# Optimization experiments

Measured on AMD Instinct MI355X. Metric: run time of the kernel, lower is better.

The kernel has to match this reference:

```python
import jax, jax.numpy as jnp
import numpy as np

B, T, C, H = 16, 2048, 768, 128

def setup_inputs() -> dict:
    key = jax.random.key(0)
    k1, k2, k3, k4 = jax.random.split(key, 4)
    x = jax.random.normal(k1, (B, T, C), dtype=jnp.float32)
    Wq = jax.random.normal(k2, (C, H), dtype=jnp.float32) * (C ** -0.5)
    Wk = jax.random.normal(k3, (C, H), dtype=jnp.float32) * (C ** -0.5)
    Wv = jax.random.normal(k4, (C, H), dtype=jnp.float32) * (C ** -0.5)
    return {"x": x, "Wq": Wq, "Wk": Wk, "Wv": Wv}

def reference(x, Wq, Wk, Wv):
    Bc, Tc, Cc = x.shape
    q = jnp.einsum('btc,ch->bth', x, Wq)
    k = jnp.einsum('btc,ch->bth', x, Wk)
    v = jnp.einsum('btc,ch->bth', x, Wv)
    wei = jnp.einsum('bqh,bkh->bqk', q, k)  # [B,T,T]
    tril = jnp.tril(jnp.ones((Tc, Tc), dtype=jnp.float32))
    # Faithful to original: mask with -inf FIRST, then scale by C**-0.5
    wei = jnp.where(tril == 0, -jnp.inf, wei) * (Cc ** -0.5)
    wei = jax.nn.softmax(wei, axis=-1)
    out = jnp.einsum('bqk,bkh->bqh', wei, v)
    return out
```

## Files before the change

kernel.cpp:

```cpp
#include <hip/hip_runtime.h>
#include <hip/hip_bf16.h>
#include <cstdint>

#define B_ 16
#define T_ 2048
#define C_ 768
#define H_ 128

typedef __bf16 bf16x8 __attribute__((ext_vector_type(8)));
typedef float f32x4 __attribute__((ext_vector_type(4)));
typedef float f32x16 __attribute__((ext_vector_type(16)));
typedef unsigned short u16x8 __attribute__((ext_vector_type(8)));
typedef unsigned int u32x4 __attribute__((ext_vector_type(4)));

__device__ __forceinline__ void gld_lds16(const void* g, void* s) {
    __builtin_amdgcn_global_load_lds(
        (__attribute__((address_space(1))) void*)(size_t)g,
        (__attribute__((address_space(3))) void*)s,
        16, 0, 0);
}

__device__ __forceinline__ unsigned short f2bf(float f) {
    __bf16 h = (__bf16)f;
    return __builtin_bit_cast(unsigned short, h);
}

__global__ __launch_bounds__(256) void wconv_kernel(
    const float* __restrict__ Wq, const float* __restrict__ Wk,
    const float* __restrict__ Wv, unsigned short* __restrict__ wT) {
    int idx = blockIdx.x * 256 + threadIdx.x;
    if (idx >= 3 * H_ * C_) return;
    int w = idx / (H_ * C_);
    int r = idx % (H_ * C_);
    int h = r / C_;
    int c = r % C_;
    const float* W = (w == 0) ? Wq : ((w == 1) ? Wk : Wv);
    wT[idx] = f2bf(W[c * H_ + h]);
}

__global__ __launch_bounds__(512, 2) void proj_kernel(
    const float* __restrict__ x, const unsigned short* __restrict__ wT,
    unsigned short* __restrict__ qb, unsigned short* __restrict__ kb,
    unsigned short* __restrict__ vtb) {
    __shared__ unsigned short Asm[2][128 * 64];
    __shared__ unsigned short Bsm[2][192 * 64];

    const int tid = threadIdx.x;
    const int nh = blockIdx.x & 1;
    const int m0 = (blockIdx.x >> 1) * 128;
    const int wid = tid >> 6;
    const int lane = tid & 63;
    const int quad = lane >> 4;
    const int lo16 = lane & 15;
    const int mh = (wid >> 2) * 64;
    const int wnl = (wid & 3) * 48;
    const unsigned short* wTn = wT + (size_t)nh * 192 * C_;

    f32x4 acc[4][3] = {};
    f32x4 pre[4];

#pragma unroll
    for (int r = 0; r < 2; ++r) {
        int cidx = r * 512 + tid;
        int m = cidx >> 3, lc = cidx & 7;
        const float* src = x + (size_t)(m0 + m) * C_ + lc * 8;
        pre[r * 2] = *(const f32x4*)src;
        pre[r * 2 + 1] = *(const f32x4*)(src + 4);
    }
    asm volatile("" ::: "memory");
#pragma unroll
    for (int r = 0; r < 3; ++r) {
        int cidx = r * 512 + tid;
        int n = cidx >> 3, c = (cidx & 7) ^ (n & 7);
        gld_lds16((const char*)wTn + ((size_t)n * C_ + c * 8) * 2,
                  (char*)&Bsm[0][0] + (r * 512 + wid * 64) * 16);
    }
    asm volatile("s_waitcnt vmcnt(3)" ::: "memory");
    __builtin_amdgcn_sched_barrier(0);
#pragma unroll
    for (int r = 0; r < 2; ++r) {
        int cidx = r * 512 + tid;
        int m = cidx >> 3, lc = cidx & 7;
        u16x8 o;
        o[0] = f2bf(pre[r * 2][0]); o[1] = f2bf(pre[r * 2][1]);
        o[2] = f2bf(pre[r * 2][2]); o[3] = f2bf(pre[r * 2][3]);
        o[4] = f2bf(pre[r * 2 + 1][0]); o[5] = f2bf(pre[r * 2 + 1][1]);
        o[6] = f2bf(pre[r * 2 + 1][2]); o[7] = f2bf(pre[r * 2 + 1][3]);
        *(u16x8*)(&Asm[0][m * 64 + (lc ^ (m & 7)) * 8]) = o;
    }
    asm volatile("s_waitcnt lgkmcnt(0)" ::: "memory");
    __builtin_amdgcn_sched_barrier(0);

    for (int kt = 0; kt < 12; ++kt) {
        const int p = kt & 1;
        __builtin_amdgcn_s_barrier();
        if (kt + 1 < 12) {
            const int k1 = (kt + 1) * 64;
#pragma unroll
            for (int r = 0; r < 2; ++r) {
                int cidx = r * 512 + tid;
                int m = cidx >> 3, lc = cidx & 7;
                const float* src = x + (size_t)(m0 + m) * C_ + k1 + lc * 8;
                pre[r * 2] = *(const f32x4*)src;
                pre[r * 2 + 1] = *(const f32x4*)(src + 4);
            }
            asm volatile("" ::: "memory");
#pragma unroll
            for (int r = 0; r < 3; ++r) {
                int cidx = r * 512 + tid;
                int n = cidx >> 3, c = (cidx & 7) ^ (n & 7);
                gld_lds16((const char*)wTn + ((size_t)n * C_ + k1 + c * 8) * 2,
                          (char*)&Bsm[p ^ 1][0] + (r * 512 + wid * 64) * 16);
            }
            asm volatile("s_waitcnt vmcnt(7)" ::: "memory");
        } else {
            asm volatile("s_waitcnt vmcnt(0)" ::: "memory");
        }
        __builtin_amdgcn_s_barrier();
        __builtin_amdgcn_sched_barrier(0);

#pragma unroll
        for (int kk = 0; kk < 2; ++kk) {
            bf16x8 af[4], bf[3];
#pragma unroll
            for (int mi = 0; mi < 4; ++mi) {
                int m = mh + mi * 16 + lo16;
                int c = (kk * 4 + quad) ^ (m & 7);
                af[mi] = *(const bf16x8*)((const __bf16*)&Asm[p][0] + m * 64 + c * 8);
            }
#pragma unroll
            for (int ni = 0; ni < 3; ++ni) {
                int n = wnl + ni * 16 + lo16;
                int c = (kk * 4 + quad) ^ (n & 7);
                bf[ni] = *(const bf16x8*)((const __bf16*)&Bsm[p][0] + n * 64 + c * 8);
            }
#pragma unroll
            for (int mi = 0; mi < 4; ++mi)
#pragma unroll
                for (int ni = 0; ni < 3; ++ni)
                    acc[mi][ni] = __builtin_amdgcn_mfma_f32_16x16x32_bf16(
                        af[mi], bf[ni], acc[mi][ni], 0, 0, 0);
        }

        if (kt + 1 < 12) {
            asm volatile("s_waitcnt vmcnt(3)" ::: "memory");
            __builtin_amdgcn_sched_barrier(0);
#pragma unroll
            for (int r = 0; r < 2; ++r) {
                int cidx = r * 512 + tid;
                int m = cidx >> 3, lc = cidx & 7;
                u16x8 o;
                o[0] = f2bf(pre[r * 2][0]); o[1] = f2bf(pre[r * 2][1]);
                o[2] = f2bf(pre[r * 2][2]); o[3] = f2bf(pre[r * 2][3]);
                o[4] = f2bf(pre[r * 2 + 1][0]); o[5] = f2bf(pre[r * 2 + 1][1]);
                o[6] = f2bf(pre[r * 2 + 1][2]); o[7] = f2bf(pre[r * 2 + 1][3]);
                *(u16x8*)(&Asm[p ^ 1][m * 64 + (lc ^ (m & 7)) * 8]) = o;
            }
            asm volatile("s_waitcnt lgkmcnt(0)" ::: "memory");
            __builtin_amdgcn_sched_barrier(0);
        }
    }

#pragma unroll
    for (int mi = 0; mi < 4; ++mi) {
        int grow = m0 + mh + mi * 16 + quad * 4;
#pragma unroll
        for (int ni = 0; ni < 3; ++ni) {
            int n = nh * 192 + wnl + ni * 16 + lo16;
            int wmat = n >> 7;
            int col = n & 127;
            if (wmat < 2) {
                unsigned short* o = (wmat == 0) ? qb : kb;
#pragma unroll
                for (int rr = 0; rr < 4; ++rr)
                    o[(size_t)(grow + rr) * H_ + col] = f2bf(acc[mi][ni][rr]);
            } else {
                int b = grow >> 11;
                int t = grow & 2047;
                ushort4 pk;
                pk.x = f2bf(acc[mi][ni][0]); pk.y = f2bf(acc[mi][ni][1]);
                pk.z = f2bf(acc[mi][ni][2]); pk.w = f2bf(acc[mi][ni][3]);
                *(ushort4*)(vtb + ((size_t)b * H_ + col) * T_ + t) = pk;
            }
        }
    }
}

__device__ __forceinline__ void attn_stage(
    const unsigned short* kB, const unsigned short* vB, int kv0, int p,
    unsigned short* Ks, unsigned short* Vs, int tid, int wid) {
#pragma unroll
    for (int rnd = 0; rnd < 4; ++rnd) {
        int cidx = rnd * 256 + tid;
        int m = cidx >> 4;
        int c = (cidx & 15) ^ (m & 15);
        gld_lds16((const char*)kB + ((size_t)(kv0 + m) * H_ + c * 8) * 2,
                  (char*)(Ks + p * 64 * 128) + (rnd * 256 + wid * 64) * 16);
    }
#pragma unroll
    for (int rnd = 0; rnd < 4; ++rnd) {
        int cidx = rnd * 256 + tid;
        int d = cidx >> 3;
        int c = (cidx & 7) ^ (d & 7);
        gld_lds16((const char*)vB + ((size_t)d * T_ + kv0 + c * 8) * 2,
                  (char*)(Vs + p * 128 * 64) + (rnd * 256 + wid * 64) * 16);
    }
}

__device__ __forceinline__ void attn_seg(
    const unsigned short* kB, const unsigned short* vB, const bf16x8 qfrag[8],
    int j0, int j1, int jmask, int qbase, float& l_part, f32x16 oacc[4],
    unsigned short* Ks, unsigned short* Vs,
    int tid, int wid, int lane, int qh, int kvh) {
    const float cs = 0.05205877694341f;
    const int l31 = lane & 31;
    const int h8 = lane >> 5;
    const int rowbase = kvh * 32 + 4 * h8;
    const int qglob = qbase + l31;

    __syncthreads();
    attn_stage(kB, vB, j0 * 64, 0, Ks, Vs, tid, wid);
    for (int j = j0; j < j1; ++j) {
        const int p = (j - j0) & 1;
        __syncthreads();
        if (j + 1 < j1) attn_stage(kB, vB, (j + 1) * 64, p ^ 1, Ks, Vs, tid, wid);

        const unsigned short* Kp = Ks + p * 64 * 128;
        const unsigned short* Vp = Vs + p * 128 * 64;

        f32x16 s = {};
        const unsigned short* Kr = Kp + (kvh * 32 + l31) * 128;
#pragma unroll
        for (int ks = 0; ks < 8; ++ks) {
            int g = (ks * 2 + h8) ^ (l31 & 15);
            bf16x8 kf = *(const bf16x8*)((const __bf16*)Kr + g * 8);
            s = __builtin_amdgcn_mfma_f32_32x32x16_bf16(kf, qfrag[ks], s, 0, 0, 0);
        }

        if (j == jmask) {
#pragma unroll
            for (int r = 0; r < 16; ++r) {
                float pv = exp2f(s[r] * cs);
                int kvg = j * 64 + rowbase + (r & 3) + 8 * (r >> 2);
                if (kvg > qglob) pv = 0.f;
                l_part += pv;
                s[r] = pv;
            }
        } else {
#pragma unroll
            for (int r = 0; r < 16; ++r) {
                float pv = exp2f(s[r] * cs);
                l_part += pv;
                s[r] = pv;
            }
        }

        unsigned int w0, w1, w2, w3, w4, w5, w6, w7;
        asm("v_cvt_pk_bf16_f32 %0, %1, %2" : "=v"(w0) : "v"(s[0]), "v"(s[1]));
        asm("v_cvt_pk_bf16_f32 %0, %1, %2" : "=v"(w1) : "v"(s[2]), "v"(s[3]));
        asm("v_cvt_pk_bf16_f32 %0, %1, %2" : "=v"(w2) : "v"(s[4]), "v"(s[5]));
        asm("v_cvt_pk_bf16_f32 %0, %1, %2" : "=v"(w3) : "v"(s[6]), "v"(s[7]));
        asm("v_cvt_pk_bf16_f32 %0, %1, %2" : "=v"(w4) : "v"(s[8]), "v"(s[9]));
        asm("v_cvt_pk_bf16_f32 %0, %1, %2" : "=v"(w5) : "v"(s[10]), "v"(s[11]));
        asm("v_cvt_pk_bf16_f32 %0, %1, %2" : "=v"(w6) : "v"(s[12]), "v"(s[13]));
        asm("v_cvt_pk_bf16_f32 %0, %1, %2" : "=v"(w7) : "v"(s[14]), "v"(s[15]));
        asm("v_permlane32_swap_b32 %0, %1" : "+v"(w0), "+v"(w2));
        asm("v_permlane32_swap_b32 %0, %1" : "+v"(w1), "+v"(w3));
        asm("v_permlane32_swap_b32 %0, %1" : "+v"(w4), "+v"(w6));
        asm("v_permlane32_swap_b32 %0, %1" : "+v"(w5), "+v"(w7));
        u32x4 a0v = {w0, w1, w2, w3};
        u32x4 a1v = {w4, w5, w6, w7};
        bf16x8 pa0 = __builtin_bit_cast(bf16x8, a0v);
        bf16x8 pa1 = __builtin_bit_cast(bf16x8, a1v);

#pragma unroll
        for (int ks2 = 0; ks2 < 2; ++ks2) {
            bf16x8 pf = (ks2 == 0) ? pa0 : pa1;
#pragma unroll
            for (int dblk = 0; dblk < 4; ++dblk) {
                int d = dblk * 32 + l31;
                int vg = (kvh * 4 + ks2 * 2 + h8) ^ (d & 7);
                bf16x8 vf = *(const bf16x8*)((const __bf16*)Vp + d * 64 + vg * 8);
                oacc[dblk] = __builtin_amdgcn_mfma_f32_32x32x16_bf16(pf, vf, oacc[dblk], 0, 0, 0);
            }
        }
    }
}

__device__ __forceinline__ void load_qfrag(const unsigned short* qB, int q0,
                                           int qh, int lane, bf16x8 qf[8]) {
    const int l31 = lane & 31, h8 = lane >> 5;
    const unsigned short* qrow = qB + (size_t)(q0 + qh * 32 + l31) * H_ + h8 * 8;
#pragma unroll
    for (int ks = 0; ks < 8; ++ks) qf[ks] = *(const bf16x8*)(qrow + ks * 16);
}

__device__ __forceinline__ void xgroup_reduce(
    float& l_part, f32x16 oacc[4], unsigned short* KsBase, float* Lred,
    int lane, int qh, int kvh) {
    l_part += __shfl_xor(l_part, 32);
    __syncthreads();
    float* base = (float*)KsBase + (size_t)(qh * 64 + lane) * 64;
    if (kvh == 1) {
#pragma unroll
        for (int dblk = 0; dblk < 4; ++dblk)
#pragma unroll
            for (int part = 0; part < 4; ++part) {
                int c = dblk * 4 + part;
                f32x4 v = {oacc[dblk][part * 4 + 0], oacc[dblk][part * 4 + 1],
                           oacc[dblk][part * 4 + 2], oacc[dblk][part * 4 + 3]};
                *(f32x4*)(base + ((c ^ (lane & 15)) * 4)) = v;
            }
        if (lane < 32) Lred[qh * 32 + lane] = l_part;
    }
    __syncthreads();
    if (kvh == 0) {
#pragma unroll
        for (int dblk = 0; dblk < 4; ++dblk)
#pragma unroll
            for (int part = 0; part < 4; ++part) {
                int c = dblk * 4 + part;
                f32x4 v = *(const f32x4*)(base + ((c ^ (lane & 15)) * 4));
                oacc[dblk][part * 4 + 0] += v[0];
                oacc[dblk][part * 4 + 1] += v[1];
                oacc[dblk][part * 4 + 2] += v[2];
                oacc[dblk][part * 4 + 3] += v[3];
            }
        l_part += Lred[qh * 32 + (lane & 31)];
    }
}

__global__ __launch_bounds__(256, 2) void attn_kernel(
    const unsigned short* __restrict__ qb, const unsigned short* __restrict__ kb,
    const unsigned short* __restrict__ vtb, float* __restrict__ out,
    float* __restrict__ pO, float* __restrict__ pL) {
    __shared__ unsigned short Ks[2][64 * 128];
    __shared__ unsigned short Vs[2][128 * 64];
    __shared__ float Lred[64];

    const int tid = threadIdx.x;
    const int bid = blockIdx.x;
    const int half = bid >> 8;
    const int slot = bid & 255;
    const int r = slot >> 4;
    const int b = slot & 15;

    const unsigned short* qB = qb + (size_t)b * T_ * H_;
    const unsigned short* kB = kb + (size_t)b * T_ * H_;
    const unsigned short* vB = vtb + (size_t)b * H_ * T_;

    const int wid = tid >> 6;
    const int lane = tid & 63;
    const int l31 = lane & 31;
    const int h8 = lane >> 5;
    const int qh = wid & 1;
    const int kvh = wid >> 1;

    const int qtb = 31 - r;
    bf16x8 qf[8];
    float l_part = 0.f;
    f32x16 oacc[4] = {};

    if (half == 0) {
        load_qfrag(qB, r * 64, qh, lane, qf);
        attn_seg(kB, vB, qf, 0, r + 1, r, r * 64 + qh * 32, l_part, oacc,
                 &Ks[0][0], &Vs[0][0], tid, wid, lane, qh, kvh);
        xgroup_reduce(l_part, oacc, &Ks[0][0], Lred, lane, qh, kvh);
        if (kvh == 0) {
            float* outb = out + (size_t)b * T_ * H_;
#pragma unroll
            for (int rr = 0; rr < 16; ++rr) {
                int ql = (rr & 3) + 8 * (rr >> 2) + 4 * h8;
                float inv = 1.0f / __shfl(l_part, ql);
                float* orow = outb + (size_t)(r * 64 + qh * 32 + ql) * H_;
#pragma unroll
                for (int dblk = 0; dblk < 4; ++dblk)
                    orow[dblk * 32 + l31] = oacc[dblk][rr] * inv;
            }
        }
        l_part = 0.f;
#pragma unroll
        for (int dblk = 0; dblk < 4; ++dblk)
#pragma unroll
            for (int e = 0; e < 16; ++e) oacc[dblk][e] = 0.f;
        load_qfrag(qB, qtb * 64, qh, lane, qf);
        attn_seg(kB, vB, qf, 0, 16 - r, -1, qtb * 64 + qh * 32, l_part, oacc,
                 &Ks[0][0], &Vs[0][0], tid, wid, lane, qh, kvh);
    } else {
        load_qfrag(qB, qtb * 64, qh, lane, qf);
        attn_seg(kB, vB, qf, 16 - r, 32 - r, qtb, qtb * 64 + qh * 32, l_part, oacc,
                 &Ks[0][0], &Vs[0][0], tid, wid, lane, qh, kvh);
    }

    xgroup_reduce(l_part, oacc, &Ks[0][0], Lred, lane, qh, kvh);
    if (kvh == 0) {
        float* myO = pO + (size_t)(half * 256 + slot) * (64 * 128);
        if (lane < 32) pL[(half * 256 + slot) * 64 + qh * 32 + lane] = l_part;
#pragma unroll
        for (int rr = 0; rr < 16; ++rr) {
            int ql = qh * 32 + (rr & 3) + 8 * (rr >> 2) + 4 * h8;
#pragma unroll
            for (int dblk = 0; dblk < 4; ++dblk)
                myO[ql * 128 + dblk * 32 + l31] = oacc[dblk][rr];
        }
    }
}

__global__ __launch_bounds__(256) void combine_kernel(
    const float* __restrict__ pO, const float* __restrict__ pL,
    float* __restrict__ out) {
    const int slot = blockIdx.x;
    const int r = slot >> 4;
    const int b = slot & 15;
    const int q0 = (31 - r) * 64;
    __shared__ float ls[64];
    const int tid = threadIdx.x;
    if (tid < 64) ls[tid] = pL[slot * 64 + tid] + pL[(256 + slot) * 64 + tid];
    __syncthreads();
    const float* O0 = pO + (size_t)slot * (64 * 128);
    const float* O1 = pO + (size_t)(256 + slot) * (64 * 128);
    float* ob = out + ((size_t)b * T_ + q0) * H_;
#pragma unroll
    for (int k = 0; k < 8; ++k) {
        int idx = (k * 256 + tid) * 4;
        f32x4 a = *(const f32x4*)(O0 + idx);
        f32x4 c = *(const f32x4*)(O1 + idx);
        float inv = 1.0f / ls[idx >> 7];
        f32x4 o;
        o[0] = (a[0] + c[0]) * inv; o[1] = (a[1] + c[1]) * inv;
        o[2] = (a[2] + c[2]) * inv; o[3] = (a[3] + c[3]) * inv;
        *(f32x4*)(ob + idx) = o;
    }
}

extern "C" void kernel_launch(void* const* d_in, const int* in_sizes, int n_in,
                              void* d_out, int out_size, void* d_ws, size_t ws_size,
                              hipStream_t stream) {
    const float* x = (const float*)d_in[0];
    const float* Wq = (const float*)d_in[1];
    const float* Wk = (const float*)d_in[2];
    const float* Wv = (const float*)d_in[3];
    float* out = (float*)d_out;

    char* ws = (char*)d_ws;
    unsigned short* wT  = (unsigned short*)ws;
    unsigned short* qb  = (unsigned short*)(ws + (1ull << 20));
    unsigned short* kb  = (unsigned short*)(ws + (9ull << 20));
    unsigned short* vtb = (unsigned short*)(ws + (17ull << 20));
    float* pO = (float*)(ws + (80ull << 20));
    float* pL = (float*)(ws + (100ull << 20));

    hipLaunchKernelGGL(wconv_kernel, dim3(1152), dim3(256), 0, stream, Wq, Wk, Wv, wT);
    hipLaunchKernelGGL(proj_kernel, dim3(512), dim3(512), 0, stream, x, wT, qb, kb, vtb);
    hipLaunchKernelGGL(attn_kernel, dim3(512), dim3(256), 0, stream, qb, kb, vtb, out, pO, pL);
    hipLaunchKernelGGL(combine_kernel, dim3(256), dim3(256), 0, stream, pO, pL, out);
}
```

Baseline: 213.8 us.

## Enlarge attention query tile to 128 rows with 8-wave blocks

Doubles the attention query tile from 64 to 128 rows per block. Blocks grow to 512 threads, with four query groups sharing each staged K/V tile, and there are half as many blocks. The causal work split, masking range, partial-output layout and combine kernel are adjusted to match. The aim is to halve K/V reloads into LDS per query, at the cost of fewer blocks (256 on a large GPU), more diagonal masked work and a bigger reduction buffer that now spans both Ks and Vs.

```diff
diff --git a/kernel.cpp b/kernel.cpp
--- a/kernel.cpp
+++ b/kernel.cpp
@@ -190,28 +190,28 @@
     const unsigned short* kB, const unsigned short* vB, int kv0, int p,
     unsigned short* Ks, unsigned short* Vs, int tid, int wid) {
 #pragma unroll
-    for (int rnd = 0; rnd < 4; ++rnd) {
-        int cidx = rnd * 256 + tid;
+    for (int rnd = 0; rnd < 2; ++rnd) {
+        int cidx = rnd * 512 + tid;
         int m = cidx >> 4;
         int c = (cidx & 15) ^ (m & 15);
         gld_lds16((const char*)kB + ((size_t)(kv0 + m) * H_ + c * 8) * 2,
-                  (char*)(Ks + p * 64 * 128) + (rnd * 256 + wid * 64) * 16);
-    }
-#pragma unroll
-    for (int rnd = 0; rnd < 4; ++rnd) {
-        int cidx = rnd * 256 + tid;
+                  (char*)(Ks + p * 64 * 128) + (rnd * 512 + wid * 64) * 16);
+    }
+#pragma unroll
+    for (int rnd = 0; rnd < 2; ++rnd) {
+        int cidx = rnd * 512 + tid;
         int d = cidx >> 3;
         int c = (cidx & 7) ^ (d & 7);
         gld_lds16((const char*)vB + ((size_t)d * T_ + kv0 + c * 8) * 2,
-                  (char*)(Vs + p * 128 * 64) + (rnd * 256 + wid * 64) * 16);
+                  (char*)(Vs + p * 128 * 64) + (rnd * 512 + wid * 64) * 16);
     }
 }
 
 __device__ __forceinline__ void attn_seg(
     const unsigned short* kB, const unsigned short* vB, const bf16x8 qfrag[8],
-    int j0, int j1, int jmask, int qbase, float& l_part, f32x16 oacc[4],
+    int j0, int j1, int maskLo, int qbase, float& l_part, f32x16 oacc[4],
     unsigned short* Ks, unsigned short* Vs,
-    int tid, int wid, int lane, int qh, int kvh) {
+    int tid, int wid, int lane, int kvh) {
     const float cs = 0.05205877694341f;
     const int l31 = lane & 31;
     const int h8 = lane >> 5;
@@ -237,7 +237,7 @@
             s = __builtin_amdgcn_mfma_f32_32x32x16_bf16(kf, qfrag[ks], s, 0, 0, 0);
         }
 
-        if (j == jmask) {
+        if (j >= maskLo) {
 #pragma unroll
             for (int r = 0; r < 16; ++r) {
                 float pv = exp2f(s[r] * cs);
@@ -288,19 +288,20 @@
 }
 
 __device__ __forceinline__ void load_qfrag(const unsigned short* qB, int q0,
-                                           int qh, int lane, bf16x8 qf[8]) {
+                                           int lane, bf16x8 qf[8]) {
     const int l31 = lane & 31, h8 = lane >> 5;
-    const unsigned short* qrow = qB + (size_t)(q0 + qh * 32 + l31) * H_ + h8 * 8;
+    const unsigned short* qrow = qB + (size_t)(q0 + l31) * H_ + h8 * 8;
 #pragma unroll
     for (int ks = 0; ks < 8; ++ks) qf[ks] = *(const bf16x8*)(qrow + ks * 16);
 }
 
 __device__ __forceinline__ void xgroup_reduce(
-    float& l_part, f32x16 oacc[4], unsigned short* KsBase, float* Lred,
-    int lane, int qh, int kvh) {
+    float& l_part, f32x16 oacc[4], unsigned short* KsBase, unsigned short* VsBase,
+    float* Lred, int lane, int qg, int kvh) {
     l_part += __shfl_xor(l_part, 32);
     __syncthreads();
-    float* base = (float*)KsBase + (size_t)(qh * 64 + lane) * 64;
+    float* red = (qg < 2) ? (float*)KsBase : (float*)VsBase;
+    float* base = red + (size_t)((qg & 1) * 64 + lane) * 64;
     if (kvh == 1) {
 #pragma unroll
         for (int dblk = 0; dblk < 4; ++dblk)
@@ -311,7 +312,7 @@
                            oacc[dblk][part * 4 + 2], oacc[dblk][part * 4 + 3]};
                 *(f32x4*)(base + ((c ^ (lane & 15)) * 4)) = v;
             }
-        if (lane < 32) Lred[qh * 32 + lane] = l_part;
+        if (lane < 32) Lred[qg * 32 + lane] = l_part;
     }
     __syncthreads();
     if (kvh == 0) {
@@ -326,22 +327,22 @@
                 oacc[dblk][part * 4 + 2] += v[2];
                 oacc[dblk][part * 4 + 3] += v[3];
             }
-        l_part += Lred[qh * 32 + (lane & 31)];
-    }
-}
-
-__global__ __launch_bounds__(256, 2) void attn_kernel(
+        l_part += Lred[qg * 32 + (lane & 31)];
+    }
+}
+
+__global__ __launch_bounds__(512, 2) void attn_kernel(
     const unsigned short* __restrict__ qb, const unsigned short* __restrict__ kb,
     const unsigned short* __restrict__ vtb, float* __restrict__ out,
     float* __restrict__ pO, float* __restrict__ pL) {
     __shared__ unsigned short Ks[2][64 * 128];
     __shared__ unsigned short Vs[2][128 * 64];
-    __shared__ float Lred[64];
+    __shared__ float Lred[128];
 
     const int tid = threadIdx.x;
     const int bid = blockIdx.x;
-    const int half = bid >> 8;
-    const int slot = bid & 255;
+    const int half = bid >> 7;
+    const int slot = bid & 127;
     const int r = slot >> 4;
     const int b = slot & 15;
 
@@ -353,26 +354,26 @@
     const int lane = tid & 63;
     const int l31 = lane & 31;
     const int h8 = lane >> 5;
-    const int qh = wid & 1;
-    const int kvh = wid >> 1;
-
-    const int qtb = 31 - r;
+    const int qg = wid & 3;
+    const int kvh = wid >> 2;
+
+    const int tb = 15 - r;
     bf16x8 qf[8];
     float l_part = 0.f;
     f32x16 oacc[4] = {};
 
     if (half == 0) {
-        load_qfrag(qB, r * 64, qh, lane, qf);
-        attn_seg(kB, vB, qf, 0, r + 1, r, r * 64 + qh * 32, l_part, oacc,
-                 &Ks[0][0], &Vs[0][0], tid, wid, lane, qh, kvh);
-        xgroup_reduce(l_part, oacc, &Ks[0][0], Lred, lane, qh, kvh);
+        load_qfrag(qB, r * 128 + qg * 32, lane, qf);
+        attn_seg(kB, vB, qf, 0, 2 * r + 2, 2 * r, r * 128 + qg * 32, l_part, oacc,
+                 &Ks[0][0], &Vs[0][0], tid, wid, lane, kvh);
+        xgroup_reduce(l_part, oacc, &Ks[0][0], &Vs[0][0], Lred, lane, qg, kvh);
         if (kvh == 0) {
             float* outb = out + (size_t)b * T_ * H_;
 #pragma unroll
             for (int rr = 0; rr < 16; ++rr) {
                 int ql = (rr & 3) + 8 * (rr >> 2) + 4 * h8;
                 float inv = 1.0f / __shfl(l_part, ql);
-                float* orow = outb + (size_t)(r * 64 + qh * 32 + ql) * H_;
+                float* orow = outb + (size_t)(r * 128 + qg * 32 + ql) * H_;
 #pragma unroll
                 for (int dblk = 0; dblk < 4; ++dblk)
                     orow[dblk * 32 + l31] = oacc[dblk][rr] * inv;
@@ -383,22 +384,24 @@
         for (int dblk = 0; dblk < 4; ++dblk)
 #pragma unroll
             for (int e = 0; e < 16; ++e) oacc[dblk][e] = 0.f;
-        load_qfrag(qB, qtb * 64, qh, lane, qf);
-        attn_seg(kB, vB, qf, 0, 16 - r, -1, qtb * 64 + qh * 32, l_part, oacc,
-                 &Ks[0][0], &Vs[0][0], tid, wid, lane, qh, kvh);
+        load_qfrag(qB, tb * 128 + qg * 32, lane, qf);
+        attn_seg(kB, vB, qf, 0, 15 - 2 * r, 999, tb * 128 + qg * 32, l_part, oacc,
+                 &Ks[0][0], &Vs[0][0], tid, wid, lane, kvh);
     } else {
-        load_qfrag(qB, qtb * 64, qh, lane, qf);
-        attn_seg(kB, vB, qf, 16 - r, 32 - r, qtb, qtb * 64 + qh * 32, l_part, oacc,
-                 &Ks[0][0], &Vs[0][0], tid, wid, lane, qh, kvh);
-    }
-
-    xgroup_reduce(l_part, oacc, &Ks[0][0], Lred, lane, qh, kvh);
+        load_qfrag(qB, tb * 128 + qg * 32, lane, qf);
+        attn_seg(kB, vB, qf, 15 - 2 * r, 32 - 2 * r, 30 - 2 * r,
+                 tb * 128 + qg * 32, l_part, oacc,
+                 &Ks[0][0], &Vs[0][0], tid, wid, lane, kvh);
+    }
+
+    xgroup_reduce(l_part, oacc, &Ks[0][0], &Vs[0][0], Lred, lane, qg, kvh);
     if (kvh == 0) {
-        float* myO = pO + (size_t)(half * 256 + slot) * (64 * 128);
-        if (lane < 32) pL[(half * 256 + slot) * 64 + qh * 32 + lane] = l_part;
+        const int slotG = half * 128 + slot;
+        float* myO = pO + (size_t)slotG * (128 * 128);
+        if (lane < 32) pL[slotG * 128 + qg * 32 + lane] = l_part;
 #pragma unroll
         for (int rr = 0; rr < 16; ++rr) {
-            int ql = qh * 32 + (rr & 3) + 8 * (rr >> 2) + 4 * h8;
+            int ql = qg * 32 + (rr & 3) + 8 * (rr >> 2) + 4 * h8;
 #pragma unroll
             for (int dblk = 0; dblk < 4; ++dblk)
                 myO[ql * 128 + dblk * 32 + l31] = oacc[dblk][rr];
@@ -412,16 +415,16 @@
     const int slot = blockIdx.x;
     const int r = slot >> 4;
     const int b = slot & 15;
-    const int q0 = (31 - r) * 64;
-    __shared__ float ls[64];
+    const int q0 = (15 - r) * 128;
+    __shared__ float ls[128];
     const int tid = threadIdx.x;
-    if (tid < 64) ls[tid] = pL[slot * 64 + tid] + pL[(256 + slot) * 64 + tid];
+    if (tid < 128) ls[tid] = pL[slot * 128 + tid] + pL[(128 + slot) * 128 + tid];
     __syncthreads();
-    const float* O0 = pO + (size_t)slot * (64 * 128);
-    const float* O1 = pO + (size_t)(256 + slot) * (64 * 128);
+    const float* O0 = pO + (size_t)slot * (128 * 128);
+    const float* O1 = pO + (size_t)(128 + slot) * (128 * 128);
     float* ob = out + ((size_t)b * T_ + q0) * H_;
 #pragma unroll
-    for (int k = 0; k < 8; ++k) {
+    for (int k = 0; k < 16; ++k) {
         int idx = (k * 256 + tid) * 4;
         f32x4 a = *(const f32x4*)(O0 + idx);
         f32x4 c = *(const f32x4*)(O1 + idx);
@@ -452,6 +455,6 @@
 
     hipLaunchKernelGGL(wconv_kernel, dim3(1152), dim3(256), 0, stream, Wq, Wk, Wv, wT);
     hipLaunchKernelGGL(proj_kernel, dim3(512), dim3(512), 0, stream, x, wT, qb, kb, vtb);
-    hipLaunchKernelGGL(attn_kernel, dim3(512), dim3(256), 0, stream, qb, kb, vtb, out, pO, pL);
-    hipLaunchKernelGGL(combine_kernel, dim3(256), dim3(256), 0, stream, pO, pL, out);
-}
+    hipLaunchKernelGGL(attn_kernel, dim3(256), dim3(512), 0, stream, qb, kb, vtb, out, pO, pL);
+    hipLaunchKernelGGL(combine_kernel, dim3(128), dim3(256), 0, stream, pO, pL, out);
+}
```

Result: no change. 214.3 us (+0.2%).

## Drop split-KV combine pass and widen projection tile to all 384 columns

Applied to the files above, without the earlier changes.

The attention kernel no longer splits the long query tile's KV range across two blocks. Each of 256 blocks now processes a paired short and long query tile and writes normalized output directly, which removes the partial-output buffers and the combine kernel launch. The projection kernel computes all 384 Q/K/V columns per block instead of half, so each x tile is loaded and converted to bf16 once. In exchange, grid sizes halve to 256 blocks, which may underfill the GPU's CUs, and the doubled accumulator and LDS use raise register and shared-memory pressure.

```diff
diff --git a/kernel.cpp b/kernel.cpp
--- a/kernel.cpp
+++ b/kernel.cpp
@@ -43,20 +43,18 @@
     unsigned short* __restrict__ qb, unsigned short* __restrict__ kb,
     unsigned short* __restrict__ vtb) {
     __shared__ unsigned short Asm[2][128 * 64];
-    __shared__ unsigned short Bsm[2][192 * 64];
+    __shared__ unsigned short Bsm[2][384 * 64];
 
     const int tid = threadIdx.x;
-    const int nh = blockIdx.x & 1;
-    const int m0 = (blockIdx.x >> 1) * 128;
+    const int m0 = blockIdx.x * 128;
     const int wid = tid >> 6;
     const int lane = tid & 63;
     const int quad = lane >> 4;
     const int lo16 = lane & 15;
     const int mh = (wid >> 2) * 64;
-    const int wnl = (wid & 3) * 48;
-    const unsigned short* wTn = wT + (size_t)nh * 192 * C_;
-
-    f32x4 acc[4][3] = {};
+    const int wnl = (wid & 3) * 96;
+
+    f32x4 acc[4][6] = {};
     f32x4 pre[4];
 
 #pragma unroll
@@ -69,13 +67,13 @@
     }
     asm volatile("" ::: "memory");
 #pragma unroll
-    for (int r = 0; r < 3; ++r) {
+    for (int r = 0; r < 6; ++r) {
         int cidx = r * 512 + tid;
         int n = cidx >> 3, c = (cidx & 7) ^ (n & 7);
-        gld_lds16((const char*)wTn + ((size_t)n * C_ + c * 8) * 2,
+        gld_lds16((const char*)wT + ((size_t)n * C_ + c * 8) * 2,
                   (char*)&Bsm[0][0] + (r * 512 + wid * 64) * 16);
     }
-    asm volatile("s_waitcnt vmcnt(3)" ::: "memory");
+    asm volatile("s_waitcnt vmcnt(6)" ::: "memory");
     __builtin_amdgcn_sched_barrier(0);
 #pragma unroll
     for (int r = 0; r < 2; ++r) {
@@ -106,13 +104,13 @@
             }
             asm volatile("" ::: "memory");
 #pragma unroll
-            for (int r = 0; r < 3; ++r) {
+            for (int r = 0; r < 6; ++r) {
                 int cidx = r * 512 + tid;
                 int n = cidx >> 3, c = (cidx & 7) ^ (n & 7);
-                gld_lds16((const char*)wTn + ((size_t)n * C_ + k1 + c * 8) * 2,
+                gld_lds16((const char*)wT + ((size_t)n * C_ + k1 + c * 8) * 2,
                           (char*)&Bsm[p ^ 1][0] + (r * 512 + wid * 64) * 16);
             }
-            asm volatile("s_waitcnt vmcnt(7)" ::: "memory");
+            asm volatile("s_waitcnt vmcnt(10)" ::: "memory");
         } else {
             asm volatile("s_waitcnt vmcnt(0)" ::: "memory");
         }
@@ -121,7 +119,7 @@
 
 #pragma unroll
         for (int kk = 0; kk < 2; ++kk) {
-            bf16x8 af[4], bf[3];
+            bf16x8 af[4], bf[6];
 #pragma unroll
             for (int mi = 0; mi < 4; ++mi) {
                 int m = mh + mi * 16 + lo16;
@@ -129,7 +127,7 @@
                 af[mi] = *(const bf16x8*)((const __bf16*)&Asm[p][0] + m * 64 + c * 8);
             }
 #pragma unroll
-            for (int ni = 0; ni < 3; ++ni) {
+            for (int ni = 0; ni < 6; ++ni) {
                 int n = wnl + ni * 16 + lo16;
                 int c = (kk * 4 + quad) ^ (n & 7);
                 bf[ni] = *(const bf16x8*)((const __bf16*)&Bsm[p][0] + n * 64 + c * 8);
@@ -137,13 +135,13 @@
 #pragma unroll
             for (int mi = 0; mi < 4; ++mi)
 #pragma unroll
-                for (int ni = 0; ni < 3; ++ni)
+                for (int ni = 0; ni < 6; ++ni)
                     acc[mi][ni] = __builtin_amdgcn_mfma_f32_16x16x32_bf16(
                         af[mi], bf[ni], acc[mi][ni], 0, 0, 0);
         }
 
         if (kt + 1 < 12) {
-            asm volatile("s_waitcnt vmcnt(3)" ::: "memory");
+            asm volatile("s_waitcnt vmcnt(6)" ::: "memory");
             __builtin_amdgcn_sched_barrier(0);
 #pragma unroll
             for (int r = 0; r < 2; ++r) {
@@ -165,8 +163,8 @@
     for (int mi = 0; mi < 4; ++mi) {
         int grow = m0 + mh + mi * 16 + quad * 4;
 #pragma unroll
-        for (int ni = 0; ni < 3; ++ni) {
-            int n = nh * 192 + wnl + ni * 16 + lo16;
+        for (int ni = 0; ni < 6; ++ni) {
+            int n = wnl + ni * 16 + lo16;
             int wmat = n >> 7;
             int col = n & 127;
             if (wmat < 2) {
@@ -330,20 +328,33 @@
     }
 }
 
+__device__ __forceinline__ void attn_writeout(
+    float* out, int b, int qt, int qh, int lane, float l_part, f32x16 oacc[4]) {
+    const int l31 = lane & 31;
+    const int h8 = lane >> 5;
+    float* outb = out + (size_t)b * T_ * H_;
+#pragma unroll
+    for (int rr = 0; rr < 16; ++rr) {
+        int ql = (rr & 3) + 8 * (rr >> 2) + 4 * h8;
+        float inv = 1.0f / __shfl(l_part, ql);
+        float* orow = outb + (size_t)(qt * 64 + qh * 32 + ql) * H_;
+#pragma unroll
+        for (int dblk = 0; dblk < 4; ++dblk)
+            orow[dblk * 32 + l31] = oacc[dblk][rr] * inv;
+    }
+}
+
 __global__ __launch_bounds__(256, 2) void attn_kernel(
     const unsigned short* __restrict__ qb, const unsigned short* __restrict__ kb,
-    const unsigned short* __restrict__ vtb, float* __restrict__ out,
-    float* __restrict__ pO, float* __restrict__ pL) {
+    const unsigned short* __restrict__ vtb, float* __restrict__ out) {
     __shared__ unsigned short Ks[2][64 * 128];
     __shared__ unsigned short Vs[2][128 * 64];
     __shared__ float Lred[64];
 
     const int tid = threadIdx.x;
     const int bid = blockIdx.x;
-    const int half = bid >> 8;
-    const int slot = bid & 255;
-    const int r = slot >> 4;
-    const int b = slot & 15;
+    const int r = bid >> 4;
+    const int b = bid & 15;
 
     const unsigned short* qB = qb + (size_t)b * T_ * H_;
     const unsigned short* kB = kb + (size_t)b * T_ * H_;
@@ -351,86 +362,30 @@
 
     const int wid = tid >> 6;
     const int lane = tid & 63;
-    const int l31 = lane & 31;
-    const int h8 = lane >> 5;
     const int qh = wid & 1;
     const int kvh = wid >> 1;
 
-    const int qtb = 31 - r;
     bf16x8 qf[8];
     float l_part = 0.f;
     f32x16 oacc[4] = {};
 
-    if (half == 0) {
-        load_qfrag(qB, r * 64, qh, lane, qf);
-        attn_seg(kB, vB, qf, 0, r + 1, r, r * 64 + qh * 32, l_part, oacc,
-                 &Ks[0][0], &Vs[0][0], tid, wid, lane, qh, kvh);
-        xgroup_reduce(l_part, oacc, &Ks[0][0], Lred, lane, qh, kvh);
-        if (kvh == 0) {
-            float* outb = out + (size_t)b * T_ * H_;
-#pragma unroll
-            for (int rr = 0; rr < 16; ++rr) {
-                int ql = (rr & 3) + 8 * (rr >> 2) + 4 * h8;
-                float inv = 1.0f / __shfl(l_part, ql);
-                float* orow = outb + (size_t)(r * 64 + qh * 32 + ql) * H_;
-#pragma unroll
-                for (int dblk = 0; dblk < 4; ++dblk)
-                    orow[dblk * 32 + l31] = oacc[dblk][rr] * inv;
-            }
-        }
-        l_part = 0.f;
-#pragma unroll
-        for (int dblk = 0; dblk < 4; ++dblk)
-#pragma unroll
-            for (int e = 0; e < 16; ++e) oacc[dblk][e] = 0.f;
-        load_qfrag(qB, qtb * 64, qh, lane, qf);
-        attn_seg(kB, vB, qf, 0, 16 - r, -1, qtb * 64 + qh * 32, l_part, oacc,
-                 &Ks[0][0], &Vs[0][0], tid, wid, lane, qh, kvh);
-    } else {
-        load_qfrag(qB, qtb * 64, qh, lane, qf);
-        attn_seg(kB, vB, qf, 16 - r, 32 - r, qtb, qtb * 64 + qh * 32, l_part, oacc,
-                 &Ks[0][0], &Vs[0][0], tid, wid, lane, qh, kvh);
-    }
-
+    load_qfrag(qB, r * 64, qh, lane, qf);
+    attn_seg(kB, vB, qf, 0, r + 1, r, r * 64 + qh * 32, l_part, oacc,
+             &Ks[0][0], &Vs[0][0], tid, wid, lane, qh, kvh);
     xgroup_reduce(l_part, oacc, &Ks[0][0], Lred, lane, qh, kvh);
-    if (kvh == 0) {
-        float* myO = pO + (size_t)(half * 256 + slot) * (64 * 128);
-        if (lane < 32) pL[(half * 256 + slot) * 64 + qh * 32 + lane] = l_part;
-#pragma unroll
-        for (int rr = 0; rr < 16; ++rr) {
-            int ql = qh * 32 + (rr & 3) + 8 * (rr >> 2) + 4 * h8;
-#pragma unroll
-            for (int dblk = 0; dblk < 4; ++dblk)
-                myO[ql * 128 + dblk * 32 + l31] = oacc[dblk][rr];
-        }
-    }
-}
-
-__global__ __launch_bounds__(256) void combine_kernel(
-    const float* __restrict__ pO, const float* __restrict__ pL,
-    float* __restrict__ out) {
-    const int slot = blockIdx.x;
-    const int r = slot >> 4;
-    const int b = slot & 15;
-    const int q0 = (31 - r) * 64;
-    __shared__ float ls[64];
-    const int tid = threadIdx.x;
-    if (tid < 64) ls[tid] = pL[slot * 64 + tid] + pL[(256 + slot) * 64 + tid];
-    __syncthreads();
-    const float* O0 = pO + (size_t)slot * (64 * 128);
-    const float* O1 = pO + (size_t)(256 + slot) * (64 * 128);
-    float* ob = out + ((size_t)b * T_ + q0) * H_;
-#pragma unroll
-    for (int k = 0; k < 8; ++k) {
-        int idx = (k * 256 + tid) * 4;
-        f32x4 a = *(const f32x4*)(O0 + idx);
-        f32x4 c = *(const f32x4*)(O1 + idx);
-        float inv = 1.0f / ls[idx >> 7];
-        f32x4 o;
-        o[0] = (a[0] + c[0]) * inv; o[1] = (a[1] + c[1]) * inv;
-        o[2] = (a[2] + c[2]) * inv; o[3] = (a[3] + c[3]) * inv;
-        *(f32x4*)(ob + idx) = o;
-    }
+    if (kvh == 0) attn_writeout(out, b, r, qh, lane, l_part, oacc);
+
+    const int qtb = 31 - r;
+    l_part = 0.f;
+#pragma unroll
+    for (int dblk = 0; dblk < 4; ++dblk)
+#pragma unroll
+        for (int e = 0; e < 16; ++e) oacc[dblk][e] = 0.f;
+    load_qfrag(qB, qtb * 64, qh, lane, qf);
+    attn_seg(kB, vB, qf, 0, 32 - r, qtb, qtb * 64 + qh * 32, l_part, oacc,
+             &Ks[0][0], &Vs[0][0], tid, wid, lane, qh, kvh);
+    xgroup_reduce(l_part, oacc, &Ks[0][0], Lred, lane, qh, kvh);
+    if (kvh == 0) attn_writeout(out, b, qtb, qh, lane, l_part, oacc);
 }
 
 extern "C" void kernel_launch(void* const* d_in, const int* in_sizes, int n_in,
@@ -447,11 +402,8 @@
     unsigned short* qb  = (unsigned short*)(ws + (1ull << 20));
     unsigned short* kb  = (unsigned short*)(ws + (9ull << 20));
     unsigned short* vtb = (unsigned short*)(ws + (17ull << 20));
-    float* pO = (float*)(ws + (80ull << 20));
-    float* pL = (float*)(ws + (100ull << 20));
 
     hipLaunchKernelGGL(wconv_kernel, dim3(1152), dim3(256), 0, stream, Wq, Wk, Wv, wT);
-    hipLaunchKernelGGL(proj_kernel, dim3(512), dim3(512), 0, stream, x, wT, qb, kb, vtb);
-    hipLaunchKernelGGL(attn_kernel, dim3(512), dim3(256), 0, stream, qb, kb, vtb, out, pO, pL);
-    hipLaunchKernelGGL(combine_kernel, dim3(256), dim3(256), 0, stream, pO, pL, out);
-}
+    hipLaunchKernelGGL(proj_kernel, dim3(256), dim3(512), 0, stream, x, wT, qb, kb, vtb);
+    hipLaunchKernelGGL(attn_kernel, dim3(256), dim3(256), 0, stream, qb, kb, vtb, out);
+}
```

Result: no change. 216.5 us (+1.2%).
